# Optimization experiments

Measured on AMD Instinct MI355X. Metric: run time of the kernel, lower is better.

## Reference

```python
import jax, jax.numpy as jnp
import numpy as np

L_F, HOP, DELTA, L_S, COND, GH = 32, 16, 3, 96, 32, 64
B, T = 128, 48000


def setup_inputs() -> dict:
    key = jax.random.key(0)
    ks = jax.random.split(key, 12)
    s = 0.05
    return {
        "x": jax.random.normal(ks[0], (B, T), jnp.float32),
        # GRU (PyTorch layout): weight_ih (3H, L_S), weight_hh (3H, H)
        "W_ih": jax.random.normal(ks[1], (3 * GH, L_S), jnp.float32) * s,
        "W_hh": jax.random.normal(ks[2], (3 * GH, GH), jnp.float32) * s,
        "b_ih": jax.random.normal(ks[3], (3 * GH,), jnp.float32) * s,
        "b_hh": jax.random.normal(ks[4], (3 * GH,), jnp.float32) * s,
        # SlowBranch output projection -> cond_dim
        "W_cs": jax.random.normal(ks[5], (COND, GH), jnp.float32) * s,
        "b_cs": jax.random.normal(ks[6], (COND,), jnp.float32) * s,
        # FastEC MLP
        "W1": jax.random.normal(ks[7], (GH, L_F + COND), jnp.float32) * s,
        "b1": jax.random.normal(ks[8], (GH,), jnp.float32) * s,
        "W2": jax.random.normal(ks[9], (L_F, GH), jnp.float32) * s,
        "b2": jax.random.normal(ks[10], (L_F,), jnp.float32) * s,
    }


def reference(x, W_ih, W_hh, b_ih, b_hh, W_cs, b_cs, W1, b1, W2, b2):
    Bsz, Tlen = x.shape
    Nf = (Tlen - L_F) // HOP + 1
    win_s = DELTA * HOP * 2
    hop_s = DELTA * HOP
    Ns = (Tlen - win_s) // hop_s + 1

    f_starts = jnp.arange(Nf) * HOP                      # (Nf,)
    fast_idx = f_starts[:, None] + jnp.arange(L_F)       # (Nf, L_F)
    fast_frames = x[:, fast_idx]                         # (B, Nf, L_F)

    s_starts = jnp.arange(Ns) * hop_s
    slow_frames = x[:, s_starts[:, None] + jnp.arange(win_s)]  # (B, Ns, L_S)

    # Single-layer GRU over slow frames (PyTorch gate order r, z, n)
    def step(h, xt):
        gi = xt @ W_ih.T + b_ih                          # (B, 3H)
        gh = h @ W_hh.T + b_hh
        i_r, i_z, i_n = jnp.split(gi, 3, axis=-1)
        h_r, h_z, h_n = jnp.split(gh, 3, axis=-1)
        r = jax.nn.sigmoid(i_r + h_r)
        z = jax.nn.sigmoid(i_z + h_z)
        n = jnp.tanh(i_n + r * h_n)
        hn = (1.0 - z) * n + z * h
        return hn, hn

    h0 = jnp.zeros((Bsz, GH), x.dtype)
    _, hs = jax.lax.scan(step, h0, jnp.swapaxes(slow_frames, 0, 1))
    hs = jnp.swapaxes(hs, 0, 1)                          # (B, Ns, GH)
    c_s = hs @ W_cs.T + b_cs                             # (B, Ns, COND)

    # per-fast-frame conditioning vector (gather)
    idx = jnp.clip(jnp.arange(Nf) // DELTA - 1, 0, None)
    c = c_s[:, idx]                                      # (B, Nf, COND)

    # FastEC batched over all frames at once
    h = jnp.concatenate([fast_frames, c], axis=-1)       # (B, Nf, L_F+COND)
    h = jax.nn.relu(h @ W1.T + b1)
    y = h @ W2.T + b2                                    # (B, Nf, L_F)

    # overlap-add scatter
    out = jnp.zeros_like(x).at[:, fast_idx].add(y)
    return out
```

## Files before the change

### kernel.cpp

```cpp
#include <hip/hip_runtime.h>

constexpr int Bn  = 128;
constexpr int Tn  = 48000;
constexpr int NFn = 2999;
constexpr int NSn = 999;
constexpr int G3n = 192;
constexpr int GHn = 64;

typedef float f2 __attribute__((ext_vector_type(2)));
typedef float f4 __attribute__((ext_vector_type(4)));

__global__ __launch_bounds__(192) void gi_kernel(const float* __restrict__ x,
                                                 const float* __restrict__ W_ih,
                                                 const float* __restrict__ b_ih,
                                                 float* __restrict__ GI) {
  __shared__ __align__(16) float WT[48 * 196];
  __shared__ __align__(16) float xs[1584];
  const int tile = blockIdx.x;
  const int b    = blockIdx.y;
  const int t0   = tile * 32;
  const int nt   = min(32, NSn - t0);
  const int tid  = threadIdx.x;

  const int span = (nt - 1) * 48 + 96;
  for (int i = tid; i < 1584; i += 192)
    xs[i] = (i < span) ? x[(size_t)b * Tn + t0 * 48 + i] : 0.0f;

  const int jq = tid % 48;
  const int tg = tid / 48;
  const int j0 = jq * 4;

  float acc[8][4];
#pragma unroll
  for (int u = 0; u < 8; ++u)
#pragma unroll
    for (int jj = 0; jj < 4; ++jj) acc[u][jj] = b_ih[j0 + jj];

  for (int half = 0; half < 2; ++half) {
    __syncthreads();
    for (int e = tid; e < 192 * 48; e += 192) {
      int j = e / 48, k = e % 48;
      WT[k * 196 + j] = W_ih[j * 96 + half * 48 + k];
    }
    __syncthreads();
    for (int kc = 0; kc < 48; kc += 4) {
      f4 wq[4];
#pragma unroll
      for (int kk = 0; kk < 4; ++kk)
        wq[kk] = *(const f4*)&WT[(kc + kk) * 196 + j0];
      f4 xq[8];
#pragma unroll
      for (int u = 0; u < 8; ++u)
        xq[u] = *(const f4*)&xs[(tg * 8 + u) * 48 + half * 48 + kc];
#pragma unroll
      for (int u = 0; u < 8; ++u) {
#pragma unroll
        for (int kk = 0; kk < 4; ++kk) {
          const float xv = xq[u][kk];
          acc[u][0] = fmaf(xv, wq[kk][0], acc[u][0]);
          acc[u][1] = fmaf(xv, wq[kk][1], acc[u][1]);
          acc[u][2] = fmaf(xv, wq[kk][2], acc[u][2]);
          acc[u][3] = fmaf(xv, wq[kk][3], acc[u][3]);
        }
      }
    }
  }

#pragma unroll
  for (int u = 0; u < 8; ++u) {
    int tl = tg * 8 + u;
    if (tl < nt) {
      float4 st = make_float4(acc[u][0], acc[u][1], acc[u][2], acc[u][3]);
      *(float4*)&GI[(size_t)(b * NSn + t0 + tl) * G3n + j0] = st;
    }
  }
}

__device__ __forceinline__ float fsigmoid(float v) {
  return __fdividef(1.0f, 1.0f + __expf(-v));
}
__device__ __forceinline__ float ftanh_f(float v) {
  return 1.0f - __fdividef(2.0f, __expf(2.0f * v) + 1.0f);
}

__device__ __forceinline__ void gru_body(const float* __restrict__ GI,
                                         const float* __restrict__ W_hh,
                                         const float* __restrict__ b_hh,
                                         float* __restrict__ hs,
                                         float* hbuf, int b, int j) {
  f2 wr2[32], wz2[32], wn2[32];
  const f2* Wr = (const f2*)(W_hh + (size_t)j * 64);
  const f2* Wz = (const f2*)(W_hh + (size_t)(j + 64) * 64);
  const f2* Wn = (const f2*)(W_hh + (size_t)(j + 128) * 64);
#pragma unroll
  for (int q = 0; q < 32; ++q) { wr2[q] = Wr[q]; wz2[q] = Wz[q]; wn2[q] = Wn[q]; }
#pragma unroll
  for (int q = 0; q < 32; ++q) {
    asm volatile("" : "+v"(wr2[q]));
    asm volatile("" : "+v"(wz2[q]));
    asm volatile("" : "+v"(wn2[q]));
  }
  const float br = b_hh[j], bz = b_hh[j + 64], bn = b_hh[j + 128];

  hbuf[j] = 0.0f;
  float hj = 0.0f;
  __builtin_amdgcn_wave_barrier();

  const float* gp = GI + (size_t)b * NSn * G3n;
  float* hsp = hs + (size_t)b * NSn * GHn;

  float pr0, pr1, pr2, pz0, pz1, pz2, pn0, pn1, pn2;
  pr0 = gp[0 * G3n + j];       pz0 = gp[0 * G3n + 64 + j];  pn0 = gp[0 * G3n + 128 + j];
  pr1 = gp[1 * G3n + j];       pz1 = gp[1 * G3n + 64 + j];  pn1 = gp[1 * G3n + 128 + j];

  for (int t = 0; t < NSn; ++t) {
    const size_t off = (size_t)min(t + 2, NSn - 1) * G3n;
    pr2 = gp[off + j];
    pz2 = gp[off + 64 + j];
    pn2 = gp[off + 128 + j];

    const f2* h2 = (const f2*)hbuf;
    f2 ar0 = {0.f, 0.f}, ar1 = {0.f, 0.f}, ar2 = {0.f, 0.f}, ar3 = {0.f, 0.f};
    f2 az0 = {0.f, 0.f}, az1 = {0.f, 0.f}, az2 = {0.f, 0.f}, az3 = {0.f, 0.f};
    f2 an0 = {0.f, 0.f}, an1 = {0.f, 0.f}, an2 = {0.f, 0.f}, an3 = {0.f, 0.f};
#pragma unroll
    for (int q = 0; q < 8; ++q) {
      f2 h0 = h2[q * 4 + 0], h1 = h2[q * 4 + 1], h2v = h2[q * 4 + 2], h3 = h2[q * 4 + 3];
      ar0 += wr2[q * 4 + 0] * h0; ar1 += wr2[q * 4 + 1] * h1;
      ar2 += wr2[q * 4 + 2] * h2v; ar3 += wr2[q * 4 + 3] * h3;
      az0 += wz2[q * 4 + 0] * h0; az1 += wz2[q * 4 + 1] * h1;
      az2 += wz2[q * 4 + 2] * h2v; az3 += wz2[q * 4 + 3] * h3;
      an0 += wn2[q * 4 + 0] * h0; an1 += wn2[q * 4 + 1] * h1;
      an2 += wn2[q * 4 + 2] * h2v; an3 += wn2[q * 4 + 3] * h3;
    }
    f2 sr = (ar0 + ar1) + (ar2 + ar3);
    f2 sz = (az0 + az1) + (az2 + az3);
    f2 sn = (an0 + an1) + (an2 + an3);

    float r = fsigmoid(pr0 + br + sr.x + sr.y);
    float z = fsigmoid(pz0 + bz + sz.x + sz.y);
    float n = ftanh_f(fmaf(r, bn + sn.x + sn.y, pn0));
    float hn = fmaf(z, hj - n, n);

    __builtin_amdgcn_wave_barrier();
    hbuf[j] = hn;
    __builtin_amdgcn_wave_barrier();
    hj = hn;
    hsp[(size_t)t * GHn + j] = hn;

    pr0 = pr1; pr1 = pr2;
    pz0 = pz1; pz1 = pz2;
    pn0 = pn1; pn1 = pn2;
  }
}

__global__ __attribute__((amdgpu_flat_work_group_size(64, 64),
                          amdgpu_waves_per_eu(1, 1),
                          amdgpu_num_vgpr(256)))
void gru_kernel(const float* __restrict__ GI,
                const float* __restrict__ W_hh,
                const float* __restrict__ b_hh,
                float* __restrict__ hs) {
  __shared__ __align__(16) float hbuf[64];
  gru_body(GI, W_hh, b_hh, hs, hbuf, blockIdx.x, threadIdx.x);
}

constexpr int UCHUNK = 125;
constexpr int NCH    = 24;

__global__ __attribute__((amdgpu_flat_work_group_size(64, 64),
                          amdgpu_waves_per_eu(1, 1),
                          amdgpu_num_vgpr(256)))
void fat_kernel(const float* __restrict__ GI,
                const float* __restrict__ W_hh,
                const float* __restrict__ b_hh,
                float* __restrict__ hs,
                const float* __restrict__ x,
                const float* __restrict__ W1,
                const float* __restrict__ b1,
                float* __restrict__ U) {
  __shared__ __align__(16) float hbuf[64];
  __shared__ __align__(16) float xs[UCHUNK * 16 + 16];
  const int tid = threadIdx.x;

  if (blockIdx.x < Bn) {
    __builtin_amdgcn_s_setprio(1);
    gru_body(GI, W_hh, b_hh, hs, hbuf, blockIdx.x, tid);
    __builtin_amdgcn_s_setprio(0);
    return;
  }

  const int ub = blockIdx.x - Bn;
  const int b  = ub / NCH;
  const int ch = ub % NCH;
  const int fA = ch * UCHUNK;
  const int fE = min(fA + UCHUNK, NFn);
  const int o  = tid;

  const int nsamp = (fE - fA - 1) * 16 + 32;
  for (int i = tid; i < nsamp; i += 64)
    xs[i] = x[(size_t)b * Tn + fA * 16 + i];

  f4 w1f[8];
#pragma unroll
  for (int i = 0; i < 8; ++i)
    w1f[i] = *(const f4*)&W1[(size_t)o * 64 + 4 * i];
  const float bo = b1[o];
  __syncthreads();

  float* Up = U + ((size_t)b * NFn) * GHn + o;
  for (int f = fA; f < fE; ++f) {
    const f4* xq = (const f4*)&xs[(f - fA) * 16];
    float a0 = bo, a1 = 0.f, a2 = 0.f, a3 = 0.f;
#pragma unroll
    for (int i = 0; i < 8; ++i) {
      f4 xv = xq[i];
      a0 = fmaf(xv[0], w1f[i][0], a0);
      a1 = fmaf(xv[1], w1f[i][1], a1);
      a2 = fmaf(xv[2], w1f[i][2], a2);
      a3 = fmaf(xv[3], w1f[i][3], a3);
    }
    Up[(size_t)f * GHn] = (a0 + a1) + (a2 + a3);
  }
}

__global__ __launch_bounds__(256) void d_kernel(const float* __restrict__ hs,
                                                const float* __restrict__ W_cs,
                                                const float* __restrict__ b_cs,
                                                const float* __restrict__ W1,
                                                float* __restrict__ d) {
  __shared__ __align__(16) float WcT[64 * 36];
  __shared__ __align__(16) float W1cT[32 * 68];
  __shared__ __align__(16) float hsl[32 * 65];
  __shared__ __align__(16) float cloc[32 * 36];
  __shared__ __align__(16) float bcs[32];
  const int tile = blockIdx.x;
  const int b    = blockIdx.y;
  const int t0   = tile * 32;
  const int nt   = min(32, NSn - t0);
  const int tid  = threadIdx.x;

  for (int e = tid; e < 32 * 64; e += 256) {
    int i = e >> 6, k = e & 63;
    WcT[k * 36 + i] = W_cs[e];
  }
  for (int e = tid; e < 64 * 32; e += 256) {
    int o = e >> 5, i = e & 31;
    W1cT[i * 68 + o] = W1[(size_t)o * 64 + 32 + i];
  }
  for (int e = tid; e < nt * 64; e += 256) {
    int t = e >> 6, k = e & 63;
    hsl[t * 65 + k] = hs[((size_t)b * NSn + t0 + t) * GHn + k];
  }
  if (tid < 32) bcs[tid] = b_cs[tid];
  __syncthreads();

  {
    const int iq = tid & 7;
    const int t  = tid >> 3;
    if (t < nt) {
      float4 acc = *(const float4*)&bcs[iq * 4];
      const float* hr = &hsl[t * 65];
#pragma unroll 4
      for (int k = 0; k < 64; ++k) {
        float hv = hr[k];
        float4 w = *(const float4*)&WcT[k * 36 + iq * 4];
        acc.x = fmaf(w.x, hv, acc.x);
        acc.y = fmaf(w.y, hv, acc.y);
        acc.z = fmaf(w.z, hv, acc.z);
        acc.w = fmaf(w.w, hv, acc.w);
      }
      *(float4*)&cloc[t * 36 + iq * 4] = acc;
    }
  }
  __syncthreads();

  for (int it = tid; it < 32 * 16; it += 256) {
    const int oq = it & 15;
    const int t  = it >> 4;
    if (t < nt) {
      float a0 = 0.f, a1 = 0.f, a2 = 0.f, a3 = 0.f;
      const float* cr = &cloc[t * 36];
#pragma unroll 4
      for (int i = 0; i < 32; ++i) {
        float cv = cr[i];
        float4 w = *(const float4*)&W1cT[i * 68 + oq * 4];
        a0 = fmaf(w.x, cv, a0);
        a1 = fmaf(w.y, cv, a1);
        a2 = fmaf(w.z, cv, a2);
        a3 = fmaf(w.w, cv, a3);
      }
      float4 st = make_float4(a0, a1, a2, a3);
      *(float4*)&d[((size_t)b * NSn + t0 + t) * GHn + oq * 4] = st;
    }
  }
}

__global__ __launch_bounds__(256) void cs_kernel(const float* __restrict__ hs,
                                                 const float* __restrict__ W_cs,
                                                 const float* __restrict__ b_cs,
                                                 float* __restrict__ cs) {
  __shared__ __align__(16) float WcT[64 * 36];
  __shared__ __align__(16) float hsl[32 * 65];
  __shared__ __align__(16) float bcs[32];
  const int tile = blockIdx.x;
  const int b    = blockIdx.y;
  const int t0   = tile * 32;
  const int nt   = min(32, NSn - t0);
  const int tid  = threadIdx.x;

  for (int e = tid; e < 32 * 64; e += 256) {
    int i = e >> 6, k = e & 63;
    WcT[k * 36 + i] = W_cs[e];
  }
  for (int e = tid; e < nt * 64; e += 256) {
    int t = e >> 6, k = e & 63;
    hsl[t * 65 + k] = hs[((size_t)b * NSn + t0 + t) * GHn + k];
  }
  if (tid < 32) bcs[tid] = b_cs[tid];
  __syncthreads();

  const int oq = tid & 7;
  const int t  = tid >> 3;
  if (t < nt) {
    float4 acc = *(const float4*)&bcs[oq * 4];
    const float* hr = &hsl[t * 65];
#pragma unroll 4
    for (int k = 0; k < 64; ++k) {
      float hv = hr[k];
      float4 w = *(const float4*)&WcT[k * 36 + oq * 4];
      acc.x = fmaf(w.x, hv, acc.x);
      acc.y = fmaf(w.y, hv, acc.y);
      acc.z = fmaf(w.z, hv, acc.z);
      acc.w = fmaf(w.w, hv, acc.w);
    }
    *(float4*)&cs[((size_t)b * NSn + t0 + t) * 32 + oq * 4] = acc;
  }
}

__global__ __launch_bounds__(256) void out2_kernel(const float* __restrict__ U,
                                                   const float* __restrict__ d,
                                                   const float* __restrict__ W2,
                                                   const float* __restrict__ b2,
                                                   float* __restrict__ out) {
  __shared__ __align__(16) float h1loc[33 * 68];
  __shared__ __align__(16) float W2T[64 * 36];
  __shared__ __align__(16) float yloc[33 * 32];
  __shared__ __align__(16) float dloc[12][68];
  __shared__ __align__(16) float bb2[32];

  const int fb  = blockIdx.x;
  const int b   = blockIdx.y;
  const int f0  = fb * 32;
  const int nf  = min(33, NFn - f0);
  const int tid = threadIdx.x;
  const int ts0 = max(f0 / 3 - 1, 0);

  for (int e = tid; e < 32 * 64; e += 256) {
    int o = e >> 6, k = e & 63;
    W2T[k * 36 + o] = W2[e];
  }
  if (tid < 32) bb2[tid] = b2[tid];
  for (int e = tid; e < 12 * 64; e += 256) {
    int ti = e >> 6, o = e & 63;
    int ts = min(ts0 + ti, NSn - 1);
    dloc[ti][o] = d[((size_t)b * NSn + ts) * GHn + o];
  }
  __syncthreads();

  for (int it = tid; it < 33 * 16; it += 256) {
    const int lf = it >> 4, oq = it & 15;
    const int f  = f0 + lf;
    f4 s = {0.f, 0.f, 0.f, 0.f};
    if (f < NFn) {
      f4 u  = *(const f4*)&U[((size_t)b * NFn + f) * GHn + oq * 4];
      const int ti = max(f / 3 - 1, 0) - ts0;
      f4 dv = *(const f4*)&dloc[ti][oq * 4];
      s = u + dv;
#pragma unroll
      for (int c = 0; c < 4; ++c) s[c] = fmaxf(s[c], 0.f);
    }
    *(f4*)&h1loc[lf * 68 + oq * 4] = s;
  }
  __syncthreads();

  for (int it = tid; it < 33 * 8; it += 256) {
    const int lf = it >> 3, oq = it & 7;
    float4 acc = *(const float4*)&bb2[oq * 4];
    const float* hr = &h1loc[lf * 68];
#pragma unroll 4
    for (int k = 0; k < 64; ++k) {
      float hv = hr[k];
      float4 w = *(const float4*)&W2T[k * 36 + oq * 4];
      acc.x = fmaf(w.x, hv, acc.x);
      acc.y = fmaf(w.y, hv, acc.y);
      acc.z = fmaf(w.z, hv, acc.z);
      acc.w = fmaf(w.w, hv, acc.w);
    }
    *(float4*)&yloc[lf * 32 + oq * 4] = acc;
  }
  __syncthreads();

  const int s0 = f0 * 16 + 16;
  const int s1 = min(s0 + 512, Tn);
  for (int s = s0 + tid; s < s1; s += 256) {
    int f1  = s >> 4;
    int o1  = s & 15;
    int lf1 = f1 - f0;
    float v = yloc[(lf1 - 1) * 32 + o1 + 16];
    if (lf1 < nf) v += yloc[lf1 * 32 + o1];
    out[(size_t)b * Tn + s] = v;
  }
  if (fb == 0 && tid < 16) out[(size_t)b * Tn + tid] = yloc[tid];
}

__global__ __launch_bounds__(256) void out_kernel(const float* __restrict__ x,
                                                  const float* __restrict__ cs,
                                                  const float* __restrict__ W1,
                                                  const float* __restrict__ b1,
                                                  const float* __restrict__ W2,
                                                  const float* __restrict__ b2,
                                                  float* __restrict__ out) {
  __shared__ __align__(16) float A[33 * 65];
  __shared__ __align__(16) float W1T[64 * 68];
  __shared__ __align__(16) float W2T[64 * 36];
  __shared__ __align__(16) float h1loc[33 * 65];
  __shared__ __align__(16) float yloc[33 * 32];
  __shared__ __align__(16) float bb1[64];
  __shared__ __align__(16) float bb2[32];

  const int fb  = blockIdx.x;
  const int b   = blockIdx.y;
  const int f0  = fb * 32;
  const int nf  = min(33, NFn - f0);
  const int tid = threadIdx.x;

  for (int e = tid; e < 64 * 64; e += 256) {
    int o = e >> 6, k = e & 63;
    W1T[k * 68 + o] = W1[e];
  }
  for (int e = tid; e < 32 * 64; e += 256) {
    int o = e >> 6, k = e & 63;
    W2T[k * 36 + o] = W2[e];
  }
  if (tid < 64) bb1[tid] = b1[tid];
  if (tid < 32) bb2[tid] = b2[tid];

  for (int e = tid; e < 33 * 32; e += 256) {
    int lf = e >> 5, k = e & 31;
    int g = (f0 + lf) * 16 + k;
    A[lf * 65 + k] = (lf < nf && g < Tn) ? x[(size_t)b * Tn + g] : 0.0f;
  }
  for (int e = tid; e < 33 * 32; e += 256) {
    int lf = e >> 5, k = e & 31;
    int ts = max((f0 + lf) / 3 - 1, 0);
    A[lf * 65 + 32 + k] = (lf < nf) ? cs[((size_t)b * NSn + ts) * 32 + k] : 0.0f;
  }
  __syncthreads();

  for (int it = tid; it < 33 * 16; it += 256) {
    int lf = it >> 4, oq = it & 15;
    float4 acc = *(const float4*)&bb1[oq * 4];
    const float* ar = &A[lf * 65];
#pragma unroll 4
    for (int k = 0; k < 64; ++k) {
      float av = ar[k];
      float4 w = *(const float4*)&W1T[k * 68 + oq * 4];
      acc.x = fmaf(w.x, av, acc.x);
      acc.y = fmaf(w.y, av, acc.y);
      acc.z = fmaf(w.z, av, acc.z);
      acc.w = fmaf(w.w, av, acc.w);
    }
    acc.x = fmaxf(acc.x, 0.0f); acc.y = fmaxf(acc.y, 0.0f);
    acc.z = fmaxf(acc.z, 0.0f); acc.w = fmaxf(acc.w, 0.0f);
    *(float4*)&h1loc[lf * 65 + oq * 4] = acc;
  }
  __syncthreads();

  for (int it = tid; it < 33 * 8; it += 256) {
    int lf = it >> 3, oq = it & 7;
    float4 acc = *(const float4*)&bb2[oq * 4];
    const float* hr = &h1loc[lf * 65];
#pragma unroll 4
    for (int k = 0; k < 64; ++k) {
      float hv = hr[k];
      float4 w = *(const float4*)&W2T[k * 36 + oq * 4];
      acc.x = fmaf(w.x, hv, acc.x);
      acc.y = fmaf(w.y, hv, acc.y);
      acc.z = fmaf(w.z, hv, acc.z);
      acc.w = fmaf(w.w, hv, acc.w);
    }
    *(float4*)&yloc[lf * 32 + oq * 4] = acc;
  }
  __syncthreads();

  const int s0 = f0 * 16 + 16;
  const int s1 = min(s0 + 512, Tn);
  for (int s = s0 + tid; s < s1; s += 256) {
    int f1  = s >> 4;
    int o1  = s & 15;
    int lf1 = f1 - f0;
    float v = yloc[(lf1 - 1) * 32 + o1 + 16];
    if (lf1 < nf) v += yloc[lf1 * 32 + o1];
    out[(size_t)b * Tn + s] = v;
  }
  if (fb == 0 && tid < 16) out[(size_t)b * Tn + tid] = yloc[tid];
}

extern "C" void kernel_launch(void* const* d_in, const int* in_sizes, int n_in,
                              void* d_out, int out_size, void* d_ws, size_t ws_size,
                              hipStream_t stream) {
  const float* x    = (const float*)d_in[0];
  const float* W_ih = (const float*)d_in[1];
  const float* W_hh = (const float*)d_in[2];
  const float* b_ih = (const float*)d_in[3];
  const float* b_hh = (const float*)d_in[4];
  const float* W_cs = (const float*)d_in[5];
  const float* b_cs = (const float*)d_in[6];
  const float* W1   = (const float*)d_in[7];
  const float* b1   = (const float*)d_in[8];
  const float* W2   = (const float*)d_in[9];
  const float* b2   = (const float*)d_in[10];
  float* out = (float*)d_out;

  const size_t giN = (size_t)Bn * NSn * G3n;
  const size_t hsN = (size_t)Bn * NSn * GHn;
  const size_t uN  = (size_t)Bn * NFn * GHn;

  float* GI = (float*)d_ws;
  float* hs = GI + giN;

  gi_kernel<<<dim3(32, Bn), 192, 0, stream>>>(x, W_ih, b_ih, GI);

  if (ws_size >= (giN + hsN + uN) * sizeof(float)) {
    float* U = hs + hsN;
    float* d = GI;
    fat_kernel<<<Bn + Bn * NCH, 64, 0, stream>>>(GI, W_hh, b_hh, hs,
                                                 x, W1, b1, U);
    d_kernel<<<dim3(32, Bn), 256, 0, stream>>>(hs, W_cs, b_cs, W1, d);
    out2_kernel<<<dim3(94, Bn), 256, 0, stream>>>(U, d, W2, b2, out);
  } else {
    float* cs = GI;
    gru_kernel<<<Bn, 64, 0, stream>>>(GI, W_hh, b_hh, hs);
    cs_kernel<<<dim3(32, Bn), 256, 0, stream>>>(hs, W_cs, b_cs, cs);
    out_kernel<<<dim3(94, Bn), 256, 0, stream>>>(x, cs, W1, b1, W2, b2, out);
  }
}
```

Baseline: 768.0 us.

## Fuse input-gate GEMM into persistent GRU kernel with per-chunk flag sync

The separate gi_kernel launch is removed. Its work moves into the fused kernel as producer blocks that each compute one 32-step chunk of one gate group and then bump a per-(batch, chunk) atomic flag. The GRU blocks spin-wait on these flags before reading each chunk of GI, so the recurrence can begin before all input projections are done. The out buffer is reused as flag storage after a memset. This overlaps the GEMM with the serial recurrence, but adds polling, fences, and a reliance on producer blocks getting scheduled while GRU blocks sit resident and spin.

```diff
diff --git a/kernel.cpp b/kernel.cpp
--- a/kernel.cpp
+++ b/kernel.cpp
@@ -10,48 +10,181 @@
 typedef float f2 __attribute__((ext_vector_type(2)));
 typedef float f4 __attribute__((ext_vector_type(4)));
 
-__global__ __launch_bounds__(192) void gi_kernel(const float* __restrict__ x,
-                                                 const float* __restrict__ W_ih,
-                                                 const float* __restrict__ b_ih,
-                                                 float* __restrict__ GI) {
-  __shared__ __align__(16) float WT[48 * 196];
-  __shared__ __align__(16) float xs[1584];
-  const int tile = blockIdx.x;
-  const int b    = blockIdx.y;
-  const int t0   = tile * 32;
-  const int nt   = min(32, NSn - t0);
-  const int tid  = threadIdx.x;
-
-  const int span = (nt - 1) * 48 + 96;
-  for (int i = tid; i < 1584; i += 192)
-    xs[i] = (i < span) ? x[(size_t)b * Tn + t0 * 48 + i] : 0.0f;
-
-  const int jq = tid % 48;
-  const int tg = tid / 48;
-  const int j0 = jq * 4;
-
-  float acc[8][4];
-#pragma unroll
-  for (int u = 0; u < 8; ++u)
-#pragma unroll
-    for (int jj = 0; jj < 4; ++jj) acc[u][jj] = b_ih[j0 + jj];
-
-  for (int half = 0; half < 2; ++half) {
-    __syncthreads();
-    for (int e = tid; e < 192 * 48; e += 192) {
-      int j = e / 48, k = e % 48;
-      WT[k * 196 + j] = W_ih[j * 96 + half * 48 + k];
-    }
-    __syncthreads();
-    for (int kc = 0; kc < 48; kc += 4) {
+__device__ __forceinline__ float fsigmoid(float v) {
+  return __fdividef(1.0f, 1.0f + __expf(-v));
+}
+__device__ __forceinline__ float ftanh_f(float v) {
+  return 1.0f - __fdividef(2.0f, __expf(2.0f * v) + 1.0f);
+}
+
+template <bool POLL>
+__device__ __forceinline__ void gru_body(const float* __restrict__ GI,
+                                         const float* __restrict__ W_hh,
+                                         const float* __restrict__ b_hh,
+                                         float* __restrict__ hs,
+                                         float* hbuf, int b, int j,
+                                         unsigned int* flags) {
+  f2 wr2[32], wz2[32], wn2[32];
+  const f2* Wr = (const f2*)(W_hh + (size_t)j * 64);
+  const f2* Wz = (const f2*)(W_hh + (size_t)(j + 64) * 64);
+  const f2* Wn = (const f2*)(W_hh + (size_t)(j + 128) * 64);
+#pragma unroll
+  for (int q = 0; q < 32; ++q) { wr2[q] = Wr[q]; wz2[q] = Wz[q]; wn2[q] = Wn[q]; }
+#pragma unroll
+  for (int q = 0; q < 32; ++q) {
+    asm volatile("" : "+v"(wr2[q]));
+    asm volatile("" : "+v"(wz2[q]));
+    asm volatile("" : "+v"(wn2[q]));
+  }
+  const float br = b_hh[j], bz = b_hh[j + 64], bn = b_hh[j + 128];
+
+  unsigned int* fl = POLL ? (flags + b * 32) : nullptr;
+  int cur_tc = 0;
+  if (POLL) {
+    if (j == 0) {
+      while (__hip_atomic_load(&fl[0], __ATOMIC_ACQUIRE,
+                               __HIP_MEMORY_SCOPE_AGENT) < 3u)
+        __builtin_amdgcn_s_sleep(4);
+    }
+    __builtin_amdgcn_wave_barrier();
+    __threadfence();
+  }
+
+  hbuf[j] = 0.0f;
+  float hj = 0.0f;
+  __builtin_amdgcn_wave_barrier();
+
+  const float* gp = GI + (size_t)b * NSn * G3n;
+  float* hsp = hs + (size_t)b * NSn * GHn;
+
+  float pr0, pr1, pr2, pz0, pz1, pz2, pn0, pn1, pn2;
+  pr0 = gp[0 * G3n + j];       pz0 = gp[0 * G3n + 64 + j];  pn0 = gp[0 * G3n + 128 + j];
+  pr1 = gp[1 * G3n + j];       pz1 = gp[1 * G3n + 64 + j];  pn1 = gp[1 * G3n + 128 + j];
+
+  for (int t = 0; t < NSn; ++t) {
+    const int tn = min(t + 2, NSn - 1);
+    if (POLL) {
+      const int tc2 = tn >> 5;
+      if (tc2 != cur_tc) {
+        if (j == 0) {
+          while (__hip_atomic_load(&fl[tc2], __ATOMIC_ACQUIRE,
+                                   __HIP_MEMORY_SCOPE_AGENT) < 3u)
+            __builtin_amdgcn_s_sleep(4);
+        }
+        __builtin_amdgcn_wave_barrier();
+        __threadfence();
+        cur_tc = tc2;
+      }
+    }
+    const size_t off = (size_t)tn * G3n;
+    pr2 = gp[off + j];
+    pz2 = gp[off + 64 + j];
+    pn2 = gp[off + 128 + j];
+
+    const f2* h2 = (const f2*)hbuf;
+    f2 ar0 = {0.f, 0.f}, ar1 = {0.f, 0.f}, ar2 = {0.f, 0.f}, ar3 = {0.f, 0.f};
+    f2 az0 = {0.f, 0.f}, az1 = {0.f, 0.f}, az2 = {0.f, 0.f}, az3 = {0.f, 0.f};
+    f2 an0 = {0.f, 0.f}, an1 = {0.f, 0.f}, an2 = {0.f, 0.f}, an3 = {0.f, 0.f};
+#pragma unroll
+    for (int q = 0; q < 8; ++q) {
+      f2 h0 = h2[q * 4 + 0], h1 = h2[q * 4 + 1], h2v = h2[q * 4 + 2], h3 = h2[q * 4 + 3];
+      ar0 += wr2[q * 4 + 0] * h0; ar1 += wr2[q * 4 + 1] * h1;
+      ar2 += wr2[q * 4 + 2] * h2v; ar3 += wr2[q * 4 + 3] * h3;
+      az0 += wz2[q * 4 + 0] * h0; az1 += wz2[q * 4 + 1] * h1;
+      az2 += wz2[q * 4 + 2] * h2v; az3 += wz2[q * 4 + 3] * h3;
+      an0 += wn2[q * 4 + 0] * h0; an1 += wn2[q * 4 + 1] * h1;
+      an2 += wn2[q * 4 + 2] * h2v; an3 += wn2[q * 4 + 3] * h3;
+    }
+    f2 sr = (ar0 + ar1) + (ar2 + ar3);
+    f2 sz = (az0 + az1) + (az2 + az3);
+    f2 sn = (an0 + an1) + (an2 + an3);
+
+    float r = fsigmoid(pr0 + br + sr.x + sr.y);
+    float z = fsigmoid(pz0 + bz + sz.x + sz.y);
+    float n = ftanh_f(fmaf(r, bn + sn.x + sn.y, pn0));
+    float hn = fmaf(z, hj - n, n);
+
+    __builtin_amdgcn_wave_barrier();
+    hbuf[j] = hn;
+    __builtin_amdgcn_wave_barrier();
+    hj = hn;
+    hsp[(size_t)t * GHn + j] = hn;
+
+    pr0 = pr1; pr1 = pr2;
+    pz0 = pz1; pz1 = pz2;
+    pn0 = pn1; pn1 = pn2;
+  }
+}
+
+constexpr int UCHUNK = 125;
+constexpr int NCH    = 24;
+constexpr int NPROD  = Bn * 32 * 3;
+
+__global__ __attribute__((amdgpu_flat_work_group_size(64, 64),
+                          amdgpu_waves_per_eu(1, 1),
+                          amdgpu_num_vgpr(256)))
+void fat3_kernel(const float* __restrict__ x,
+                 const float* __restrict__ W_ih,
+                 const float* __restrict__ b_ih,
+                 const float* __restrict__ W_hh,
+                 const float* __restrict__ b_hh,
+                 const float* __restrict__ W1,
+                 const float* __restrict__ b1,
+                 float* __restrict__ GI,
+                 float* __restrict__ hs,
+                 float* __restrict__ U,
+                 unsigned int* __restrict__ flags) {
+  __shared__ __align__(16) float smem[8112];
+  const int tid = threadIdx.x;
+
+  if (blockIdx.x < Bn) {
+    __builtin_amdgcn_s_setprio(1);
+    gru_body<true>(GI, W_hh, b_hh, hs, smem, blockIdx.x, tid, flags);
+    __builtin_amdgcn_s_setprio(0);
+    return;
+  }
+
+  if (blockIdx.x < Bn + NPROD) {
+    const int pid = blockIdx.x - Bn;
+    const int tc  = pid / (Bn * 3);
+    const int rr  = pid - tc * (Bn * 3);
+    const int b   = rr / 3;
+    const int g   = rr - b * 3;
+    float* WT = smem;
+    float* xs = smem + 6528;
+
+    const int nt   = min(32, NSn - tc * 32);
+    const int span = (nt - 1) * 48 + 96;
+    for (int i = tid; i < 1584; i += 64)
+      xs[i] = (i < span) ? x[(size_t)b * Tn + (size_t)tc * 1536 + i] : 0.0f;
+    for (int e4 = tid * 4; e4 < 64 * 96; e4 += 64 * 4) {
+      f4 v = *(const f4*)&W_ih[(size_t)g * 64 * 96 + e4];
+      const int row = e4 / 96, k = e4 - row * 96;
+#pragma unroll
+      for (int c = 0; c < 4; ++c) WT[(k + c) * 68 + row] = v[c];
+    }
+    __builtin_amdgcn_wave_barrier();
+    asm volatile("s_waitcnt lgkmcnt(0)" ::: "memory");
+
+    const int jq = tid & 15;
+    const int tg = tid >> 4;
+    const int j0 = jq * 4;
+
+    float acc[8][4];
+#pragma unroll
+    for (int u = 0; u < 8; ++u)
+#pragma unroll
+      for (int jj = 0; jj < 4; ++jj) acc[u][jj] = b_ih[g * 64 + j0 + jj];
+
+    for (int kc = 0; kc < 96; kc += 4) {
       f4 wq[4];
 #pragma unroll
       for (int kk = 0; kk < 4; ++kk)
-        wq[kk] = *(const f4*)&WT[(kc + kk) * 196 + j0];
+        wq[kk] = *(const f4*)&WT[(kc + kk) * 68 + j0];
       f4 xq[8];
 #pragma unroll
       for (int u = 0; u < 8; ++u)
-        xq[u] = *(const f4*)&xs[(tg * 8 + u) * 48 + half * 48 + kc];
+        xq[u] = *(const f4*)&xs[(tg * 8 + u) * 48 + kc];
 #pragma unroll
       for (int u = 0; u < 8; ++u) {
 #pragma unroll
@@ -64,157 +197,48 @@
         }
       }
     }
-  }
-
-#pragma unroll
-  for (int u = 0; u < 8; ++u) {
-    int tl = tg * 8 + u;
-    if (tl < nt) {
-      float4 st = make_float4(acc[u][0], acc[u][1], acc[u][2], acc[u][3]);
-      *(float4*)&GI[(size_t)(b * NSn + t0 + tl) * G3n + j0] = st;
-    }
-  }
-}
-
-__device__ __forceinline__ float fsigmoid(float v) {
-  return __fdividef(1.0f, 1.0f + __expf(-v));
-}
-__device__ __forceinline__ float ftanh_f(float v) {
-  return 1.0f - __fdividef(2.0f, __expf(2.0f * v) + 1.0f);
-}
-
-__device__ __forceinline__ void gru_body(const float* __restrict__ GI,
-                                         const float* __restrict__ W_hh,
-                                         const float* __restrict__ b_hh,
-                                         float* __restrict__ hs,
-                                         float* hbuf, int b, int j) {
-  f2 wr2[32], wz2[32], wn2[32];
-  const f2* Wr = (const f2*)(W_hh + (size_t)j * 64);
-  const f2* Wz = (const f2*)(W_hh + (size_t)(j + 64) * 64);
-  const f2* Wn = (const f2*)(W_hh + (size_t)(j + 128) * 64);
-#pragma unroll
-  for (int q = 0; q < 32; ++q) { wr2[q] = Wr[q]; wz2[q] = Wz[q]; wn2[q] = Wn[q]; }
-#pragma unroll
-  for (int q = 0; q < 32; ++q) {
-    asm volatile("" : "+v"(wr2[q]));
-    asm volatile("" : "+v"(wz2[q]));
-    asm volatile("" : "+v"(wn2[q]));
-  }
-  const float br = b_hh[j], bz = b_hh[j + 64], bn = b_hh[j + 128];
-
-  hbuf[j] = 0.0f;
-  float hj = 0.0f;
-  __builtin_amdgcn_wave_barrier();
-
-  const float* gp = GI + (size_t)b * NSn * G3n;
-  float* hsp = hs + (size_t)b * NSn * GHn;
-
-  float pr0, pr1, pr2, pz0, pz1, pz2, pn0, pn1, pn2;
-  pr0 = gp[0 * G3n + j];       pz0 = gp[0 * G3n + 64 + j];  pn0 = gp[0 * G3n + 128 + j];
-  pr1 = gp[1 * G3n + j];       pz1 = gp[1 * G3n + 64 + j];  pn1 = gp[1 * G3n + 128 + j];
-
-  for (int t = 0; t < NSn; ++t) {
-    const size_t off = (size_t)min(t + 2, NSn - 1) * G3n;
-    pr2 = gp[off + j];
-    pz2 = gp[off + 64 + j];
-    pn2 = gp[off + 128 + j];
-
-    const f2* h2 = (const f2*)hbuf;
-    f2 ar0 = {0.f, 0.f}, ar1 = {0.f, 0.f}, ar2 = {0.f, 0.f}, ar3 = {0.f, 0.f};
-    f2 az0 = {0.f, 0.f}, az1 = {0.f, 0.f}, az2 = {0.f, 0.f}, az3 = {0.f, 0.f};
-    f2 an0 = {0.f, 0.f}, an1 = {0.f, 0.f}, an2 = {0.f, 0.f}, an3 = {0.f, 0.f};
-#pragma unroll
-    for (int q = 0; q < 8; ++q) {
-      f2 h0 = h2[q * 4 + 0], h1 = h2[q * 4 + 1], h2v = h2[q * 4 + 2], h3 = h2[q * 4 + 3];
-      ar0 += wr2[q * 4 + 0] * h0; ar1 += wr2[q * 4 + 1] * h1;
-      ar2 += wr2[q * 4 + 2] * h2v; ar3 += wr2[q * 4 + 3] * h3;
-      az0 += wz2[q * 4 + 0] * h0; az1 += wz2[q * 4 + 1] * h1;
-      az2 += wz2[q * 4 + 2] * h2v; az3 += wz2[q * 4 + 3] * h3;
-      an0 += wn2[q * 4 + 0] * h0; an1 += wn2[q * 4 + 1] * h1;
-      an2 += wn2[q * 4 + 2] * h2v; an3 += wn2[q * 4 + 3] * h3;
-    }
-    f2 sr = (ar0 + ar1) + (ar2 + ar3);
-    f2 sz = (az0 + az1) + (az2 + az3);
-    f2 sn = (an0 + an1) + (an2 + an3);
-
-    float r = fsigmoid(pr0 + br + sr.x + sr.y);
-    float z = fsigmoid(pz0 + bz + sz.x + sz.y);
-    float n = ftanh_f(fmaf(r, bn + sn.x + sn.y, pn0));
-    float hn = fmaf(z, hj - n, n);
-
-    __builtin_amdgcn_wave_barrier();
-    hbuf[j] = hn;
-    __builtin_amdgcn_wave_barrier();
-    hj = hn;
-    hsp[(size_t)t * GHn + j] = hn;
-
-    pr0 = pr1; pr1 = pr2;
-    pz0 = pz1; pz1 = pz2;
-    pn0 = pn1; pn1 = pn2;
-  }
-}
-
-__global__ __attribute__((amdgpu_flat_work_group_size(64, 64),
-                          amdgpu_waves_per_eu(1, 1),
-                          amdgpu_num_vgpr(256)))
-void gru_kernel(const float* __restrict__ GI,
-                const float* __restrict__ W_hh,
-                const float* __restrict__ b_hh,
-                float* __restrict__ hs) {
-  __shared__ __align__(16) float hbuf[64];
-  gru_body(GI, W_hh, b_hh, hs, hbuf, blockIdx.x, threadIdx.x);
-}
-
-constexpr int UCHUNK = 125;
-constexpr int NCH    = 24;
-
-__global__ __attribute__((amdgpu_flat_work_group_size(64, 64),
-                          amdgpu_waves_per_eu(1, 1),
-                          amdgpu_num_vgpr(256)))
-void fat_kernel(const float* __restrict__ GI,
-                const float* __restrict__ W_hh,
-                const float* __restrict__ b_hh,
-                float* __restrict__ hs,
-                const float* __restrict__ x,
-                const float* __restrict__ W1,
-                const float* __restrict__ b1,
-                float* __restrict__ U) {
-  __shared__ __align__(16) float hbuf[64];
-  __shared__ __align__(16) float xs[UCHUNK * 16 + 16];
-  const int tid = threadIdx.x;
-
-  if (blockIdx.x < Bn) {
-    __builtin_amdgcn_s_setprio(1);
-    gru_body(GI, W_hh, b_hh, hs, hbuf, blockIdx.x, tid);
-    __builtin_amdgcn_s_setprio(0);
+
+#pragma unroll
+    for (int u = 0; u < 8; ++u) {
+      const int tl = tg * 8 + u;
+      if (tl < nt) {
+        float4 st = make_float4(acc[u][0], acc[u][1], acc[u][2], acc[u][3]);
+        *(float4*)&GI[(size_t)(b * NSn + tc * 32 + tl) * G3n + g * 64 + j0] = st;
+      }
+    }
+    __threadfence();
+    if (tid == 0)
+      __hip_atomic_fetch_add(&flags[b * 32 + tc], 1u, __ATOMIC_RELEASE,
+                             __HIP_MEMORY_SCOPE_AGENT);
     return;
   }
 
-  const int ub = blockIdx.x - Bn;
+  const int ub = blockIdx.x - Bn - NPROD;
   const int b  = ub / NCH;
   const int ch = ub % NCH;
   const int fA = ch * UCHUNK;
   const int fE = min(fA + UCHUNK, NFn);
-  const int o  = tid;
+  float* xu = smem;
 
   const int nsamp = (fE - fA - 1) * 16 + 32;
   for (int i = tid; i < nsamp; i += 64)
-    xs[i] = x[(size_t)b * Tn + fA * 16 + i];
+    xu[i] = x[(size_t)b * Tn + fA * 16 + i];
 
   f4 w1f[8];
 #pragma unroll
   for (int i = 0; i < 8; ++i)
-    w1f[i] = *(const f4*)&W1[(size_t)o * 64 + 4 * i];
-  const float bo = b1[o];
-  __syncthreads();
-
-  float* Up = U + ((size_t)b * NFn) * GHn + o;
+    w1f[i] = *(const f4*)&W1[(size_t)tid * 64 + 4 * i];
+  const float bo = b1[tid];
+  __builtin_amdgcn_wave_barrier();
+  asm volatile("s_waitcnt lgkmcnt(0)" ::: "memory");
+
+  float* Up = U + ((size_t)b * NFn) * GHn + tid;
   for (int f = fA; f < fE; ++f) {
-    const f4* xq = (const f4*)&xs[(f - fA) * 16];
+    const f4* xq2 = (const f4*)&xu[(f - fA) * 16];
     float a0 = bo, a1 = 0.f, a2 = 0.f, a3 = 0.f;
 #pragma unroll
     for (int i = 0; i < 8; ++i) {
-      f4 xv = xq[i];
+      f4 xv = xq2[i];
       a0 = fmaf(xv[0], w1f[i][0], a0);
       a1 = fmaf(xv[1], w1f[i][1], a1);
       a2 = fmaf(xv[2], w1f[i][2], a2);
@@ -296,6 +320,149 @@
   }
 }
 
+__global__ __launch_bounds__(256) void out2_kernel(const float* __restrict__ U,
+                                                   const float* __restrict__ d,
+                                                   const float* __restrict__ W2,
+                                                   const float* __restrict__ b2,
+                                                   float* __restrict__ out) {
+  __shared__ __align__(16) float h1loc[33 * 68];
+  __shared__ __align__(16) float W2T[64 * 36];
+  __shared__ __align__(16) float yloc[33 * 32];
+  __shared__ __align__(16) float dloc[12][68];
+  __shared__ __align__(16) float bb2[32];
+
+  const int fb  = blockIdx.x;
+  const int b   = blockIdx.y;
+  const int f0  = fb * 32;
+  const int nf  = min(33, NFn - f0);
+  const int tid = threadIdx.x;
+  const int ts0 = max(f0 / 3 - 1, 0);
+
+  for (int e = tid; e < 32 * 64; e += 256) {
+    int o = e >> 6, k = e & 63;
+    W2T[k * 36 + o] = W2[e];
+  }
+  if (tid < 32) bb2[tid] = b2[tid];
+  for (int e = tid; e < 12 * 64; e += 256) {
+    int ti = e >> 6, o = e & 63;
+    int ts = min(ts0 + ti, NSn - 1);
+    dloc[ti][o] = d[((size_t)b * NSn + ts) * GHn + o];
+  }
+  __syncthreads();
+
+  for (int it = tid; it < 33 * 16; it += 256) {
+    const int lf = it >> 4, oq = it & 15;
+    const int f  = f0 + lf;
+    f4 s = {0.f, 0.f, 0.f, 0.f};
+    if (f < NFn) {
+      f4 u  = *(const f4*)&U[((size_t)b * NFn + f) * GHn + oq * 4];
+      const int ti = max(f / 3 - 1, 0) - ts0;
+      f4 dv = *(const f4*)&dloc[ti][oq * 4];
+      s = u + dv;
+#pragma unroll
+      for (int c = 0; c < 4; ++c) s[c] = fmaxf(s[c], 0.f);
+    }
+    *(f4*)&h1loc[lf * 68 + oq * 4] = s;
+  }
+  __syncthreads();
+
+  for (int it = tid; it < 33 * 8; it += 256) {
+    const int lf = it >> 3, oq = it & 7;
+    float4 acc = *(const float4*)&bb2[oq * 4];
+    const float* hr = &h1loc[lf * 68];
+#pragma unroll 4
+    for (int k = 0; k < 64; ++k) {
+      float hv = hr[k];
+      float4 w = *(const float4*)&W2T[k * 36 + oq * 4];
+      acc.x = fmaf(w.x, hv, acc.x);
+      acc.y = fmaf(w.y, hv, acc.y);
+      acc.z = fmaf(w.z, hv, acc.z);
+      acc.w = fmaf(w.w, hv, acc.w);
+    }
+    *(float4*)&yloc[lf * 32 + oq * 4] = acc;
+  }
+  __syncthreads();
+
+  const int s0 = f0 * 16 + 16;
+  const int s1 = min(s0 + 512, Tn);
+  for (int s = s0 + tid; s < s1; s += 256) {
+    int f1  = s >> 4;
+    int o1  = s & 15;
+    int lf1 = f1 - f0;
+    float v = yloc[(lf1 - 1) * 32 + o1 + 16];
+    if (lf1 < nf) v += yloc[lf1 * 32 + o1];
+    out[(size_t)b * Tn + s] = v;
+  }
+  if (fb == 0 && tid < 16) out[(size_t)b * Tn + tid] = yloc[tid];
+}
+
+__global__ __launch_bounds__(192) void gi_kernel(const float* __restrict__ x,
+                                                 const float* __restrict__ W_ih,
+                                                 const float* __restrict__ b_ih,
+                                                 float* __restrict__ GI) {
+  __shared__ __align__(16) float WT[48 * 196];
+  __shared__ __align__(16) float xs[1584];
+  const int tile = blockIdx.x;
+  const int b    = blockIdx.y;
+  const int t0   = tile * 32;
+  const int nt   = min(32, NSn - t0);
+  const int tid  = threadIdx.x;
+
+  const int span = (nt - 1) * 48 + 96;
+  for (int i = tid; i < 1584; i += 192)
+    xs[i] = (i < span) ? x[(size_t)b * Tn + t0 * 48 + i] : 0.0f;
+
+  const int jq = tid % 48;
+  const int tg = tid / 48;
+  const int j0 = jq * 4;
+
+  float acc[8][4];
+#pragma unroll
+  for (int u = 0; u < 8; ++u)
+#pragma unroll
+    for (int jj = 0; jj < 4; ++jj) acc[u][jj] = b_ih[j0 + jj];
+
+  for (int half = 0; half < 2; ++half) {
+    __syncthreads();
+    for (int e = tid; e < 192 * 48; e += 192) {
+      int j = e / 48, k = e % 48;
+      WT[k * 196 + j] = W_ih[j * 96 + half * 48 + k];
+    }
+    __syncthreads();
+    for (int k = 0; k < 48; ++k) {
+      float4 w = *(const float4*)&WT[k * 196 + j0];
+#pragma unroll
+      for (int u = 0; u < 8; ++u) {
+        float xv = xs[(tg * 8 + u) * 48 + half * 48 + k];
+        acc[u][0] = fmaf(xv, w.x, acc[u][0]);
+        acc[u][1] = fmaf(xv, w.y, acc[u][1]);
+        acc[u][2] = fmaf(xv, w.z, acc[u][2]);
+        acc[u][3] = fmaf(xv, w.w, acc[u][3]);
+      }
+    }
+  }
+
+#pragma unroll
+  for (int u = 0; u < 8; ++u) {
+    int tl = tg * 8 + u;
+    if (tl < nt) {
+      float4 st = make_float4(acc[u][0], acc[u][1], acc[u][2], acc[u][3]);
+      *(float4*)&GI[(size_t)(b * NSn + t0 + tl) * G3n + j0] = st;
+    }
+  }
+}
+
+__global__ __attribute__((amdgpu_flat_work_group_size(64, 64),
+                          amdgpu_waves_per_eu(1, 1),
+                          amdgpu_num_vgpr(256)))
+void gru_kernel(const float* __restrict__ GI,
+                const float* __restrict__ W_hh,
+                const float* __restrict__ b_hh,
+                float* __restrict__ hs) {
+  __shared__ __align__(16) float hbuf[64];
+  gru_body<false>(GI, W_hh, b_hh, hs, hbuf, blockIdx.x, threadIdx.x, nullptr);
+}
+
 __global__ __launch_bounds__(256) void cs_kernel(const float* __restrict__ hs,
                                                  const float* __restrict__ W_cs,
                                                  const float* __restrict__ b_cs,
@@ -336,82 +503,6 @@
     }
     *(float4*)&cs[((size_t)b * NSn + t0 + t) * 32 + oq * 4] = acc;
   }
-}
-
-__global__ __launch_bounds__(256) void out2_kernel(const float* __restrict__ U,
-                                                   const float* __restrict__ d,
-                                                   const float* __restrict__ W2,
-                                                   const float* __restrict__ b2,
-                                                   float* __restrict__ out) {
-  __shared__ __align__(16) float h1loc[33 * 68];
-  __shared__ __align__(16) float W2T[64 * 36];
-  __shared__ __align__(16) float yloc[33 * 32];
-  __shared__ __align__(16) float dloc[12][68];
-  __shared__ __align__(16) float bb2[32];
-
-  const int fb  = blockIdx.x;
-  const int b   = blockIdx.y;
-  const int f0  = fb * 32;
-  const int nf  = min(33, NFn - f0);
-  const int tid = threadIdx.x;
-  const int ts0 = max(f0 / 3 - 1, 0);
-
-  for (int e = tid; e < 32 * 64; e += 256) {
-    int o = e >> 6, k = e & 63;
-    W2T[k * 36 + o] = W2[e];
-  }
-  if (tid < 32) bb2[tid] = b2[tid];
-  for (int e = tid; e < 12 * 64; e += 256) {
-    int ti = e >> 6, o = e & 63;
-    int ts = min(ts0 + ti, NSn - 1);
-    dloc[ti][o] = d[((size_t)b * NSn + ts) * GHn + o];
-  }
-  __syncthreads();
-
-  for (int it = tid; it < 33 * 16; it += 256) {
-    const int lf = it >> 4, oq = it & 15;
-    const int f  = f0 + lf;
-    f4 s = {0.f, 0.f, 0.f, 0.f};
-    if (f < NFn) {
-      f4 u  = *(const f4*)&U[((size_t)b * NFn + f) * GHn + oq * 4];
-      const int ti = max(f / 3 - 1, 0) - ts0;
-      f4 dv = *(const f4*)&dloc[ti][oq * 4];
-      s = u + dv;
-#pragma unroll
-      for (int c = 0; c < 4; ++c) s[c] = fmaxf(s[c], 0.f);
-    }
-    *(f4*)&h1loc[lf * 68 + oq * 4] = s;
-  }
-  __syncthreads();
-
-  for (int it = tid; it < 33 * 8; it += 256) {
-    const int lf = it >> 3, oq = it & 7;
-    float4 acc = *(const float4*)&bb2[oq * 4];
-    const float* hr = &h1loc[lf * 68];
-#pragma unroll 4
-    for (int k = 0; k < 64; ++k) {
-      float hv = hr[k];
-      float4 w = *(const float4*)&W2T[k * 36 + oq * 4];
-      acc.x = fmaf(w.x, hv, acc.x);
-      acc.y = fmaf(w.y, hv, acc.y);
-      acc.z = fmaf(w.z, hv, acc.z);
-      acc.w = fmaf(w.w, hv, acc.w);
-    }
-    *(float4*)&yloc[lf * 32 + oq * 4] = acc;
-  }
-  __syncthreads();
-
-  const int s0 = f0 * 16 + 16;
-  const int s1 = min(s0 + 512, Tn);
-  for (int s = s0 + tid; s < s1; s += 256) {
-    int f1  = s >> 4;
-    int o1  = s & 15;
-    int lf1 = f1 - f0;
-    float v = yloc[(lf1 - 1) * 32 + o1 + 16];
-    if (lf1 < nf) v += yloc[lf1 * 32 + o1];
-    out[(size_t)b * Tn + s] = v;
-  }
-  if (fb == 0 && tid < 16) out[(size_t)b * Tn + tid] = yloc[tid];
 }
 
 __global__ __launch_bounds__(256) void out_kernel(const float* __restrict__ x,
@@ -530,17 +621,19 @@
   float* GI = (float*)d_ws;
   float* hs = GI + giN;
 
-  gi_kernel<<<dim3(32, Bn), 192, 0, stream>>>(x, W_ih, b_ih, GI);
-
   if (ws_size >= (giN + hsN + uN) * sizeof(float)) {
     float* U = hs + hsN;
     float* d = GI;
-    fat_kernel<<<Bn + Bn * NCH, 64, 0, stream>>>(GI, W_hh, b_hh, hs,
-                                                 x, W1, b1, U);
+    unsigned int* flags = (unsigned int*)out;
+    hipMemsetAsync(out, 0, (size_t)Bn * 32 * sizeof(unsigned int), stream);
+
+    fat3_kernel<<<Bn + NPROD + Bn * NCH, 64, 0, stream>>>(
+        x, W_ih, b_ih, W_hh, b_hh, W1, b1, GI, hs, U, flags);
     d_kernel<<<dim3(32, Bn), 256, 0, stream>>>(hs, W_cs, b_cs, W1, d);
     out2_kernel<<<dim3(94, Bn), 256, 0, stream>>>(U, d, W2, b2, out);
   } else {
     float* cs = GI;
+    gi_kernel<<<dim3(32, Bn), 192, 0, stream>>>(x, W_ih, b_ih, GI);
     gru_kernel<<<Bn, 64, 0, stream>>>(GI, W_hh, b_hh, hs);
     cs_kernel<<<dim3(32, Bn), 256, 0, stream>>>(hs, W_cs, b_cs, cs);
     out_kernel<<<dim3(94, Bn), 256, 0, stream>>>(x, cs, W1, b1, W2, b2, out);
```

After: 1.247 ms. 1.62x slower.
